# Kernel optimization log

Hardware: AMD Instinct MI355X
Metric: run time of the kernel (lower is better)

## Reference

```python
import jax, jax.numpy as jnp
import numpy as np

N_HEAD = 8
N_FEAT = 256
CHUNK = 64          # window/chunk size N
D_K = N_FEAT // N_HEAD
SCALE = D_K ** (-0.5)
B_ = 2048           # batch * nChunkNum
NCHUNK = 128        # nChunkNum (B_ % NCHUNK == 0)


def setup_inputs() -> dict:
    key = jax.random.key(0)
    ks = jax.random.split(key, 12)
    f32 = jnp.float32
    query = jax.random.normal(ks[0], (B_, CHUNK, N_FEAT), f32)
    key_t = jax.random.normal(ks[1], (B_, CHUNK, N_FEAT), f32)
    value = jax.random.normal(ks[2], (B_, CHUNK, N_FEAT), f32)
    # padding mask (B_, time2): multiplicative 0/1 floats
    mask = jax.random.randint(ks[3], (B_, CHUNK), 0, 2).astype(f32)
    # shifted-chunk additive mask (nChunkNum, N, N): 0 for neighbors, -100 otherwise
    cm_bin = jax.random.randint(ks[4], (NCHUNK, CHUNK, CHUNK), 0, 2)
    chunk_mask = jnp.where(cm_bin == 1, 0.0, -100.0).astype(f32)
    def lin(k):
        return jax.random.normal(k, (N_FEAT, N_FEAT), f32) * 0.02
    Wq, Wk, Wv, Wo = lin(ks[5]), lin(ks[6]), lin(ks[7]), lin(ks[8])
    bq = jnp.zeros((N_FEAT,), f32)
    bk = jnp.zeros((N_FEAT,), f32)
    bv = jnp.zeros((N_FEAT,), f32)
    bo = jnp.zeros((N_FEAT,), f32)
    rpb_table = jax.random.normal(ks[9], (2 * CHUNK - 1, N_HEAD), f32) * 0.02
    return {"query": query, "key": key_t, "value": value, "mask": mask,
            "chunk_mask": chunk_mask, "Wq": Wq, "bq": bq, "Wk": Wk, "bk": bk,
            "Wv": Wv, "bv": bv, "Wo": Wo, "bo": bo, "rpb_table": rpb_table}


def _rel_pos_index():
    # index[i, j] = (i - j) + CHUNK - 1, shape (N, N)
    w = jnp.arange(CHUNK)
    return w[:, None] - w[None, :] + (CHUNK - 1)


def reference(query, key, value, mask, chunk_mask, Wq, bq, Wk, bk, Wv, bv, Wo, bo, rpb_table):
    B, N, _ = query.shape
    # qkv projections -> (B, h, N, d_k)
    def proj(x, W, b):
        y = x @ W.T + b
        return y.reshape(B, N, N_HEAD, D_K).transpose(0, 2, 1, 3)
    q = proj(query, Wq, bq)
    k = proj(key, Wk, bk)
    v = proj(value, Wv, bv)
    # windowed attention scores (B, h, N, N)
    scores = jnp.einsum("bhid,bhjd->bhij", q, k) * SCALE
    # relative position bias: gather (N, N, h) -> (h, N, N)
    rpb = rpb_table[_rel_pos_index()].transpose(2, 0, 1)
    scores = scores + rpb[None]
    # padding mask: multiply, then fill zeros with -100 (as in torch source)
    scores = scores * mask[:, None, None, :]
    scores = jnp.where(scores == 0, jnp.float32(-100.0), scores)
    # additive shifted-chunk mask
    nC = chunk_mask.shape[0]
    scores = scores.reshape(B // nC, nC, N_HEAD, N, N) + chunk_mask[None, :, None]
    scores = scores.reshape(B, N_HEAD, N, N)
    attn = jax.nn.softmax(scores, axis=-1)
    x = jnp.einsum("bhij,bhjd->bhid", attn, v)          # (B, h, N, d_k)
    x = x.transpose(0, 2, 1, 3).reshape(B, N, N_FEAT)     # (B, N, n_feat)
    return x @ Wo.T + bo
```

## Files before the change

kernel.cpp:

```cpp
#include <hip/hip_runtime.h>
#include <hip/hip_bf16.h>

typedef __bf16 bf16_t;
typedef __bf16 bf16x8 __attribute__((ext_vector_type(8)));
typedef __bf16 bf16x4 __attribute__((ext_vector_type(4)));
typedef float f32x4 __attribute__((ext_vector_type(4)));

#define OFF_A   0
#define OFF_B   32768
#define OFF_RPB 65536
#define OFF_CMM (65536 + 4096)
#define OFF_PAD (65536 + 4096 + 512)
#define SMEM_BYTES (65536 + 4096 + 512 + 8)

__device__ __forceinline__ int tile_off(int r, int c) {
  return (r << 9) + ((((c >> 3) ^ (r & 7)) << 4) | ((c & 7) << 1));
}
__device__ __forceinline__ int vt_off(int d, int j) {
  return (d << 7) + ((((j >> 3) ^ (d & 7)) << 4) | ((j & 7) << 1));
}
__device__ __forceinline__ int ps_off(int i, int j) {
  return (i << 6) + ((((j >> 3) ^ ((i >> 1) & 3)) << 4) | ((j & 7) << 1));
}

template <int UNROLL>
__device__ __forceinline__ void stage_x(const float* __restrict__ src, char* __restrict__ dst, int tid) {
  const float4* s4 = (const float4*)src;
#pragma unroll
  for (int kk = 0; kk < 8; kk += UNROLL) {
    float4 v[UNROLL];
#pragma unroll
    for (int u = 0; u < UNROLL; ++u) v[u] = s4[tid + ((kk + u) << 9)];
#pragma unroll
    for (int u = 0; u < UNROLL; ++u) {
      int f = tid + ((kk + u) << 9);
      int row = f >> 6;
      int col = (f & 63) << 2;
      bf16x4 p;
      p[0] = (bf16_t)v[u].x; p[1] = (bf16_t)v[u].y; p[2] = (bf16_t)v[u].z; p[3] = (bf16_t)v[u].w;
      *(bf16x4*)(dst + tile_off(row, col)) = p;
    }
  }
}

__device__ __forceinline__ void gemm_tile(const char* __restrict__ sA, const bf16_t* __restrict__ W,
                                          int cb, int l15, int g, f32x4 acc[4][2]) {
#pragma unroll
  for (int kt = 0; kt < 8; ++kt) {
    bf16x8 a[4];
#pragma unroll
    for (int mt = 0; mt < 4; ++mt)
      a[mt] = *(const bf16x8*)(sA + tile_off(mt*16 + l15, kt*32 + g*8));
#pragma unroll
    for (int nt = 0; nt < 2; ++nt) {
      bf16x8 bw = *(const bf16x8*)(W + (cb + nt*16 + l15)*256 + kt*32 + g*8);
#pragma unroll
      for (int mt = 0; mt < 4; ++mt)
        acc[mt][nt] = __builtin_amdgcn_mfma_f32_16x16x32_bf16(a[mt], bw, acc[mt][nt], 0, 0, 0);
    }
  }
}

__device__ __forceinline__ void gemm_tile2(const char* __restrict__ sA, const char* __restrict__ sB,
                                           const bf16_t* __restrict__ W0, const bf16_t* __restrict__ W1,
                                           int cb, int l15, int g,
                                           f32x4 acc0[4][2], f32x4 acc1[4][2]) {
  const bf16_t* w0p = W0 + (cb + l15)*256 + g*8;
  const bf16_t* w1p = W1 + (cb + l15)*256 + g*8;
#pragma unroll
  for (int kt = 0; kt < 8; ++kt) {
    bf16x8 a0[4], a1[4];
#pragma unroll
    for (int mt = 0; mt < 4; ++mt) {
      a0[mt] = *(const bf16x8*)(sA + tile_off(mt*16 + l15, kt*32 + g*8));
      a1[mt] = *(const bf16x8*)(sB + tile_off(mt*16 + l15, kt*32 + g*8));
    }
#pragma unroll
    for (int nt = 0; nt < 2; ++nt) {
      bf16x8 bw0 = *(const bf16x8*)(w0p + nt*16*256 + kt*32);
      bf16x8 bw1 = *(const bf16x8*)(w1p + nt*16*256 + kt*32);
#pragma unroll
      for (int mt = 0; mt < 4; ++mt) {
        acc0[mt][nt] = __builtin_amdgcn_mfma_f32_16x16x32_bf16(a0[mt], bw0, acc0[mt][nt], 0, 0, 0);
        acc1[mt][nt] = __builtin_amdgcn_mfma_f32_16x16x32_bf16(a1[mt], bw1, acc1[mt][nt], 0, 0, 0);
      }
    }
  }
}

__global__ __launch_bounds__(512, 2)
void chunk_attn_kernel(
    const float* __restrict__ qg, const float* __restrict__ kg, const float* __restrict__ vg,
    const float* __restrict__ maskg, const float* __restrict__ cmg,
    const float* __restrict__ bq, const float* __restrict__ bk, const float* __restrict__ bv,
    const float* __restrict__ bo, const float* __restrict__ rpbg,
    const bf16_t* __restrict__ Wb, float* __restrict__ outg) {
  extern __shared__ char sm[];
  char*  bufA  = sm + OFF_A;
  char*  bufB  = sm + OFF_B;
  float* sRpb  = (float*)(sm + OFF_RPB);
  char*  sCmm  = sm + OFF_CMM;

  const int b = blockIdx.x, tid = threadIdx.x;
  const int wave = tid >> 6, lane = tid & 63, l15 = lane & 15, g = lane >> 4;
  const int cb = wave << 5;
  char* scr = bufB + (wave << 12);

  for (int i = tid; i < 1016; i += 512) sRpb[((i & 7) << 7) + (i >> 3)] = rpbg[i];
  {
    if (wave == 0) {
      float mv = maskg[(b << 6) + lane];
      unsigned long long bm = __ballot(mv == 0.0f);
      if (lane == 0) *(unsigned long long*)(sm + OFF_PAD) = bm;
    }
    const float* cmb = cmg + ((size_t)(b & 127) << 12);
#pragma unroll
    for (int it = 0; it < 8; ++it) {
      int row = (wave << 3) + it;
      float cv = cmb[(row << 6) + lane];
      unsigned long long bm = __ballot(cv < -50.0f);
      if (lane == 0) *(unsigned long long*)(sCmm + (row << 3)) = bm;
    }
  }
  stage_x<4>(qg + (size_t)b*16384, bufA, tid);
  stage_x<4>(kg + (size_t)b*16384, bufB, tid);
  __syncthreads();

  {
    f32x4 qacc[4][2] = {}, kacc[4][2] = {};
    gemm_tile2(bufA, bufB, Wb + 0*65536, Wb + 1*65536, cb, l15, g, qacc, kacc);
    __syncthreads();
    float bq0 = bq[cb+l15], bq1 = bq[cb+16+l15];
    float bk0 = bk[cb+l15], bk1 = bk[cb+16+l15];
#pragma unroll
    for (int mt = 0; mt < 4; ++mt)
#pragma unroll
      for (int nt = 0; nt < 2; ++nt)
#pragma unroll
        for (int r = 0; r < 4; ++r) {
          int row = mt*16 + g*4 + r, col = cb + nt*16 + l15;
          *(bf16_t*)(bufA + tile_off(row, col)) = (bf16_t)(qacc[mt][nt][r] + (nt ? bq1 : bq0));
          *(bf16_t*)(bufB + tile_off(row, col)) = (bf16_t)(kacc[mt][nt][r] + (nt ? bk1 : bk0));
        }
  }
  __asm__ volatile("s_waitcnt lgkmcnt(0)" ::: "memory");

  f32x4 St[4][4];
  {
    bf16x8 ka[4], qb[4];
#pragma unroll
    for (int t = 0; t < 4; ++t) {
      ka[t] = *(const bf16x8*)(bufB + tile_off(t*16 + l15, cb + g*8));
      qb[t] = *(const bf16x8*)(bufA + tile_off(t*16 + l15, cb + g*8));
    }
    const f32x4 z = {};
#pragma unroll
    for (int mj = 0; mj < 4; ++mj)
#pragma unroll
      for (int ni = 0; ni < 4; ++ni)
        St[mj][ni] = __builtin_amdgcn_mfma_f32_16x16x32_bf16(ka[mj], qb[ni], z, 0, 0, 0);
  }

  const float* rpbw = sRpb + (wave << 7);
  unsigned long long padm = *(const unsigned long long*)(sm + OFF_PAD);
  unsigned int padl = (unsigned int)padm, padh = (unsigned int)(padm >> 32);
#pragma unroll
  for (int mj = 0; mj < 4; ++mj) {
    unsigned int pw = (mj >= 2) ? padh : padl;
#pragma unroll
    for (int ni = 0; ni < 4; ++ni) {
      int i = ni*16 + l15;
      unsigned long long cmm = *(const unsigned long long*)(sCmm + (i << 3));
      unsigned int cw = (mj >= 2) ? (unsigned int)(cmm >> 32) : (unsigned int)cmm;
#pragma unroll
      for (int r = 0; r < 4; ++r) {
        int j = mj*16 + g*4 + r;
        int sh = j & 31;
        float s1 = St[mj][ni][r] * 0.17677669529663689f + rpbw[i - j + 63];
        float base = ((pw >> sh) & 1u) ? -100.0f : s1;
        St[mj][ni][r] = ((cw >> sh) & 1u) ? base - 100.0f : base;
      }
    }
  }

  float rinv[4];
  bf16x4 pbf[4][4];
#pragma unroll
  for (int ni = 0; ni < 4; ++ni) {
    float m = -1e30f;
#pragma unroll
    for (int mj = 0; mj < 4; ++mj)
#pragma unroll
      for (int r = 0; r < 4; ++r) m = fmaxf(m, St[mj][ni][r]);
    m = fmaxf(m, __shfl_xor(m, 16));
    m = fmaxf(m, __shfl_xor(m, 32));
    float s = 0.0f;
#pragma unroll
    for (int mj = 0; mj < 4; ++mj)
#pragma unroll
      for (int r = 0; r < 4; ++r) {
        float p = __expf(St[mj][ni][r] - m);
        pbf[mj][ni][r] = (bf16_t)p;
        s += p;
      }
    s += __shfl_xor(s, 16);
    s += __shfl_xor(s, 32);
    rinv[ni] = 1.0f / s;
  }

  __syncthreads();
  stage_x<4>(vg + (size_t)b*16384, bufB, tid);
  __syncthreads();

  {
    f32x4 vacc[4][2] = {};
    gemm_tile(bufB, Wb + 2*65536, cb, l15, g, vacc);
    float b0 = bv[cb+l15], b1 = bv[cb+16+l15];
#pragma unroll
    for (int nt = 0; nt < 2; ++nt)
#pragma unroll
      for (int mt = 0; mt < 4; ++mt) {
        bf16x4 p;
#pragma unroll
        for (int r = 0; r < 4; ++r) p[r] = (bf16_t)(vacc[mt][nt][r] + (nt ? b1 : b0));
        *(bf16x4*)(bufA + vt_off(cb + nt*16 + l15, mt*16 + g*4)) = p;
      }
  }
  __syncthreads();

  f32x4 Xa[2][4] = {};
#pragma unroll
  for (int h2 = 0; h2 < 2; ++h2) {
#pragma unroll
    for (int mj = 2*h2; mj < 2*h2 + 2; ++mj)
#pragma unroll
      for (int ni = 0; ni < 4; ++ni)
        *(bf16x4*)(scr + ps_off(ni*16 + l15, (mj & 1)*16 + g*4)) = pbf[mj][ni];
    __asm__ volatile("s_waitcnt lgkmcnt(0)" ::: "memory");
    bf16x8 va[2], pb[4];
#pragma unroll
    for (int mtd = 0; mtd < 2; ++mtd)
      va[mtd] = *(const bf16x8*)(bufA + vt_off(cb + mtd*16 + l15, h2*32 + g*8));
#pragma unroll
    for (int ni = 0; ni < 4; ++ni)
      pb[ni] = *(const bf16x8*)(scr + ps_off(ni*16 + l15, g*8));
#pragma unroll
    for (int mtd = 0; mtd < 2; ++mtd)
#pragma unroll
      for (int ni = 0; ni < 4; ++ni)
        Xa[mtd][ni] = __builtin_amdgcn_mfma_f32_16x16x32_bf16(va[mtd], pb[ni], Xa[mtd][ni], 0, 0, 0);
  }

  __syncthreads();
#pragma unroll
  for (int mtd = 0; mtd < 2; ++mtd)
#pragma unroll
    for (int ni = 0; ni < 4; ++ni)
#pragma unroll
      for (int r = 0; r < 4; ++r) {
        int dloc = mtd*16 + g*4 + r;
        int i = ni*16 + l15;
        *(bf16_t*)(bufB + tile_off(i, cb + dloc)) = (bf16_t)(Xa[mtd][ni][r] * rinv[ni]);
      }
  __syncthreads();

  {
    f32x4 acc[4][2] = {};
    gemm_tile(bufB, Wb + 3*65536, cb, l15, g, acc);
    float b0 = bo[cb+l15], b1 = bo[cb+16+l15];
    float* ob = outg + (size_t)b * 16384;
#pragma unroll
    for (int mt = 0; mt < 4; ++mt)
#pragma unroll
      for (int nt = 0; nt < 2; ++nt)
#pragma unroll
        for (int r = 0; r < 4; ++r)
          ob[(mt*16 + g*4 + r)*256 + cb + nt*16 + l15] = acc[mt][nt][r] + (nt ? b1 : b0);
  }
}

__global__ void cvt_weights(const float* __restrict__ Wq, const float* __restrict__ Wk,
                            const float* __restrict__ Wv, const float* __restrict__ Wo,
                            bf16_t* __restrict__ dst) {
  int idx = blockIdx.x * 256 + threadIdx.x;
  int which = idx >> 14;
  int off = idx & 16383;
  const float* src = (which == 0) ? Wq : (which == 1) ? Wk : (which == 2) ? Wv : Wo;
  float4 v = ((const float4*)src)[off];
  bf16x4 p;
  p[0] = (bf16_t)v.x; p[1] = (bf16_t)v.y; p[2] = (bf16_t)v.z; p[3] = (bf16_t)v.w;
  *(bf16x4*)(dst + which*65536 + off*4) = p;
}

extern "C" void kernel_launch(void* const* d_in, const int* in_sizes, int n_in,
                              void* d_out, int out_size, void* d_ws, size_t ws_size,
                              hipStream_t stream) {
  (void)in_sizes; (void)n_in; (void)out_size; (void)ws_size;
  const float* qg  = (const float*)d_in[0];
  const float* kg  = (const float*)d_in[1];
  const float* vg  = (const float*)d_in[2];
  const float* mg  = (const float*)d_in[3];
  const float* cmg = (const float*)d_in[4];
  const float* Wq  = (const float*)d_in[5];
  const float* bq  = (const float*)d_in[6];
  const float* Wk  = (const float*)d_in[7];
  const float* bk  = (const float*)d_in[8];
  const float* Wv  = (const float*)d_in[9];
  const float* bv  = (const float*)d_in[10];
  const float* Wo  = (const float*)d_in[11];
  const float* bo  = (const float*)d_in[12];
  const float* rpb = (const float*)d_in[13];
  bf16_t* Wb = (bf16_t*)d_ws;
  float* outg = (float*)d_out;

  hipFuncSetAttribute(reinterpret_cast<const void*>(chunk_attn_kernel),
                      hipFuncAttributeMaxDynamicSharedMemorySize, SMEM_BYTES);
  cvt_weights<<<256, 256, 0, stream>>>(Wq, Wk, Wv, Wo, Wb);
  chunk_attn_kernel<<<2048, 512, SMEM_BYTES, stream>>>(qg, kg, vg, mg, cmg,
      bq, bk, bv, bo, rpb, Wb, outg);
}
```

Measured before the change: 251.8 us.

## Fuse V projection into the QKV GEMM using a third LDS buffer

Stages Q, K and V into three separate LDS tiles up front and computes all three projections in one fused three-way GEMM loop, storing V transposed into its own buffer. This removes the later V staging phase, its separate GEMM and two block-wide barriers, and drops a barrier before the output write by moving the per-wave P scratch into the Q buffer. In exchange LDS use grows by 32 KB per block and the fused loop holds three accumulator sets at once. That likely prevents two 512-thread blocks from sharing a CU and raises register pressure.

```diff
diff --git a/kernel.cpp b/kernel.cpp
--- a/kernel.cpp
+++ b/kernel.cpp
@@ -8,10 +8,11 @@
 
 #define OFF_A   0
 #define OFF_B   32768
-#define OFF_RPB 65536
-#define OFF_CMM (65536 + 4096)
-#define OFF_PAD (65536 + 4096 + 512)
-#define SMEM_BYTES (65536 + 4096 + 512 + 8)
+#define OFF_C   65536
+#define OFF_RPB 98304
+#define OFF_CMM (98304 + 4096)
+#define OFF_PAD (98304 + 4096 + 512)
+#define SMEM_BYTES (98304 + 4096 + 512 + 8)
 
 __device__ __forceinline__ int tile_off(int r, int c) {
   return (r << 9) + ((((c >> 3) ^ (r & 7)) << 4) | ((c & 7) << 1));
@@ -45,6 +46,7 @@
 
 __device__ __forceinline__ void gemm_tile(const char* __restrict__ sA, const bf16_t* __restrict__ W,
                                           int cb, int l15, int g, f32x4 acc[4][2]) {
+  const bf16_t* wp = W + (cb + l15) * 256 + g * 8;
 #pragma unroll
   for (int kt = 0; kt < 8; ++kt) {
     bf16x8 a[4];
@@ -53,7 +55,7 @@
       a[mt] = *(const bf16x8*)(sA + tile_off(mt*16 + l15, kt*32 + g*8));
 #pragma unroll
     for (int nt = 0; nt < 2; ++nt) {
-      bf16x8 bw = *(const bf16x8*)(W + (cb + nt*16 + l15)*256 + kt*32 + g*8);
+      bf16x8 bw = *(const bf16x8*)(wp + nt * 16 * 256 + kt * 32);
 #pragma unroll
       for (int mt = 0; mt < 4; ++mt)
         acc[mt][nt] = __builtin_amdgcn_mfma_f32_16x16x32_bf16(a[mt], bw, acc[mt][nt], 0, 0, 0);
@@ -61,28 +63,35 @@
   }
 }
 
-__device__ __forceinline__ void gemm_tile2(const char* __restrict__ sA, const char* __restrict__ sB,
+__device__ __forceinline__ void gemm_tile3(const char* __restrict__ sA, const char* __restrict__ sB,
+                                           const char* __restrict__ sC,
                                            const bf16_t* __restrict__ W0, const bf16_t* __restrict__ W1,
+                                           const bf16_t* __restrict__ W2,
                                            int cb, int l15, int g,
-                                           f32x4 acc0[4][2], f32x4 acc1[4][2]) {
-  const bf16_t* w0p = W0 + (cb + l15)*256 + g*8;
-  const bf16_t* w1p = W1 + (cb + l15)*256 + g*8;
+                                           f32x4 acc0[4][2], f32x4 acc1[4][2], f32x4 acc2[4][2]) {
+  const bf16_t* w0p = W0 + (cb + l15) * 256 + g * 8;
+  const bf16_t* w1p = W1 + (cb + l15) * 256 + g * 8;
+  const bf16_t* w2p = W2 + (cb + l15) * 256 + g * 8;
 #pragma unroll
   for (int kt = 0; kt < 8; ++kt) {
-    bf16x8 a0[4], a1[4];
+    bf16x8 a0[4], a1[4], a2[4];
 #pragma unroll
     for (int mt = 0; mt < 4; ++mt) {
-      a0[mt] = *(const bf16x8*)(sA + tile_off(mt*16 + l15, kt*32 + g*8));
-      a1[mt] = *(const bf16x8*)(sB + tile_off(mt*16 + l15, kt*32 + g*8));
+      int off = tile_off(mt*16 + l15, kt*32 + g*8);
+      a0[mt] = *(const bf16x8*)(sA + off);
+      a1[mt] = *(const bf16x8*)(sB + off);
+      a2[mt] = *(const bf16x8*)(sC + off);
     }
 #pragma unroll
     for (int nt = 0; nt < 2; ++nt) {
-      bf16x8 bw0 = *(const bf16x8*)(w0p + nt*16*256 + kt*32);
-      bf16x8 bw1 = *(const bf16x8*)(w1p + nt*16*256 + kt*32);
+      bf16x8 bw0 = *(const bf16x8*)(w0p + nt * 16 * 256 + kt * 32);
+      bf16x8 bw1 = *(const bf16x8*)(w1p + nt * 16 * 256 + kt * 32);
+      bf16x8 bw2 = *(const bf16x8*)(w2p + nt * 16 * 256 + kt * 32);
 #pragma unroll
       for (int mt = 0; mt < 4; ++mt) {
         acc0[mt][nt] = __builtin_amdgcn_mfma_f32_16x16x32_bf16(a0[mt], bw0, acc0[mt][nt], 0, 0, 0);
         acc1[mt][nt] = __builtin_amdgcn_mfma_f32_16x16x32_bf16(a1[mt], bw1, acc1[mt][nt], 0, 0, 0);
+        acc2[mt][nt] = __builtin_amdgcn_mfma_f32_16x16x32_bf16(a2[mt], bw2, acc2[mt][nt], 0, 0, 0);
       }
     }
   }
@@ -98,13 +107,14 @@
   extern __shared__ char sm[];
   char*  bufA  = sm + OFF_A;
   char*  bufB  = sm + OFF_B;
+  char*  bufC  = sm + OFF_C;
   float* sRpb  = (float*)(sm + OFF_RPB);
   char*  sCmm  = sm + OFF_CMM;
 
   const int b = blockIdx.x, tid = threadIdx.x;
   const int wave = tid >> 6, lane = tid & 63, l15 = lane & 15, g = lane >> 4;
   const int cb = wave << 5;
-  char* scr = bufB + (wave << 12);
+  char* scr = bufA + (wave << 12);
 
   for (int i = tid; i < 1016; i += 512) sRpb[((i & 7) << 7) + (i >> 3)] = rpbg[i];
   {
@@ -124,11 +134,13 @@
   }
   stage_x<4>(qg + (size_t)b*16384, bufA, tid);
   stage_x<4>(kg + (size_t)b*16384, bufB, tid);
+  stage_x<4>(vg + (size_t)b*16384, bufC, tid);
   __syncthreads();
 
   {
-    f32x4 qacc[4][2] = {}, kacc[4][2] = {};
-    gemm_tile2(bufA, bufB, Wb + 0*65536, Wb + 1*65536, cb, l15, g, qacc, kacc);
+    f32x4 qacc[4][2] = {}, kacc[4][2] = {}, vacc[4][2] = {};
+    gemm_tile3(bufA, bufB, bufC, Wb + 0*65536, Wb + 1*65536, Wb + 2*65536,
+               cb, l15, g, qacc, kacc, vacc);
     __syncthreads();
     float bq0 = bq[cb+l15], bq1 = bq[cb+16+l15];
     float bk0 = bk[cb+l15], bk1 = bk[cb+16+l15];
@@ -142,6 +154,16 @@
           *(bf16_t*)(bufA + tile_off(row, col)) = (bf16_t)(qacc[mt][nt][r] + (nt ? bq1 : bq0));
           *(bf16_t*)(bufB + tile_off(row, col)) = (bf16_t)(kacc[mt][nt][r] + (nt ? bk1 : bk0));
         }
+    float bv0 = bv[cb+l15], bv1 = bv[cb+16+l15];
+#pragma unroll
+    for (int nt = 0; nt < 2; ++nt)
+#pragma unroll
+      for (int mt = 0; mt < 4; ++mt) {
+        bf16x4 p;
+#pragma unroll
+        for (int r = 0; r < 4; ++r) p[r] = (bf16_t)(vacc[mt][nt][r] + (nt ? bv1 : bv0));
+        *(bf16x4*)(bufC + vt_off(cb + nt*16 + l15, mt*16 + g*4)) = p;
+      }
   }
   __asm__ volatile("s_waitcnt lgkmcnt(0)" ::: "memory");
 
@@ -209,24 +231,6 @@
   }
 
   __syncthreads();
-  stage_x<4>(vg + (size_t)b*16384, bufB, tid);
-  __syncthreads();
-
-  {
-    f32x4 vacc[4][2] = {};
-    gemm_tile(bufB, Wb + 2*65536, cb, l15, g, vacc);
-    float b0 = bv[cb+l15], b1 = bv[cb+16+l15];
-#pragma unroll
-    for (int nt = 0; nt < 2; ++nt)
-#pragma unroll
-      for (int mt = 0; mt < 4; ++mt) {
-        bf16x4 p;
-#pragma unroll
-        for (int r = 0; r < 4; ++r) p[r] = (bf16_t)(vacc[mt][nt][r] + (nt ? b1 : b0));
-        *(bf16x4*)(bufA + vt_off(cb + nt*16 + l15, mt*16 + g*4)) = p;
-      }
-  }
-  __syncthreads();
 
   f32x4 Xa[2][4] = {};
 #pragma unroll
@@ -240,7 +244,7 @@
     bf16x8 va[2], pb[4];
 #pragma unroll
     for (int mtd = 0; mtd < 2; ++mtd)
-      va[mtd] = *(const bf16x8*)(bufA + vt_off(cb + mtd*16 + l15, h2*32 + g*8));
+      va[mtd] = *(const bf16x8*)(bufC + vt_off(cb + mtd*16 + l15, h2*32 + g*8));
 #pragma unroll
     for (int ni = 0; ni < 4; ++ni)
       pb[ni] = *(const bf16x8*)(scr + ps_off(ni*16 + l15, g*8));
@@ -251,7 +255,6 @@
         Xa[mtd][ni] = __builtin_amdgcn_mfma_f32_16x16x32_bf16(va[mtd], pb[ni], Xa[mtd][ni], 0, 0, 0);
   }
 
-  __syncthreads();
 #pragma unroll
   for (int mtd = 0; mtd < 2; ++mtd)
 #pragma unroll
```

Result: slower. 282.2 us (+12.1%).

## Split each head across two waves, doubling block size to 1024 threads

Applied to the files above, without the earlier changes.

Each head is now handled by two waves, each covering half of the rows (M tiles for the projections, query rows for attention), and the block grows from 512 to 1024 threads. Per-wave accumulators and register arrays shrink by half, which raises wave-level parallelism and should lower register pressure. In exchange, weight fragments are loaded twice per block (once by each wave of a pair), the cross-wave dependency on Q/K needs an extra full barrier in place of a waitcnt, and each wave's scratch region shrinks. Occupancy with 1024-thread blocks and 70KB of shared memory may be limited to one or two blocks per CU.

```diff
diff --git a/kernel.cpp b/kernel.cpp
--- a/kernel.cpp
+++ b/kernel.cpp
@@ -23,72 +23,68 @@
   return (i << 6) + ((((j >> 3) ^ ((i >> 1) & 3)) << 4) | ((j & 7) << 1));
 }
 
-template <int UNROLL>
 __device__ __forceinline__ void stage_x(const float* __restrict__ src, char* __restrict__ dst, int tid) {
   const float4* s4 = (const float4*)src;
 #pragma unroll
-  for (int kk = 0; kk < 8; kk += UNROLL) {
-    float4 v[UNROLL];
-#pragma unroll
-    for (int u = 0; u < UNROLL; ++u) v[u] = s4[tid + ((kk + u) << 9)];
-#pragma unroll
-    for (int u = 0; u < UNROLL; ++u) {
-      int f = tid + ((kk + u) << 9);
-      int row = f >> 6;
-      int col = (f & 63) << 2;
-      bf16x4 p;
-      p[0] = (bf16_t)v[u].x; p[1] = (bf16_t)v[u].y; p[2] = (bf16_t)v[u].z; p[3] = (bf16_t)v[u].w;
-      *(bf16x4*)(dst + tile_off(row, col)) = p;
-    }
-  }
-}
-
-__device__ __forceinline__ void gemm_tile(const char* __restrict__ sA, const bf16_t* __restrict__ W,
-                                          int cb, int l15, int g, f32x4 acc[4][2]) {
+  for (int k = 0; k < 4; ++k) {
+    int f = tid + (k << 10);
+    float4 v = s4[f];
+    int row = f >> 6;
+    int col = (f & 63) << 2;
+    bf16x4 p;
+    p[0] = (bf16_t)v.x; p[1] = (bf16_t)v.y; p[2] = (bf16_t)v.z; p[3] = (bf16_t)v.w;
+    *(bf16x4*)(dst + tile_off(row, col)) = p;
+  }
+}
+
+__device__ __forceinline__ void gemm_tileH(const char* __restrict__ sA, const bf16_t* __restrict__ W,
+                                           int cb, int mb, int l15, int g, f32x4 acc[2][2]) {
+  const bf16_t* wp = W + (cb + l15)*256 + g*8;
 #pragma unroll
   for (int kt = 0; kt < 8; ++kt) {
-    bf16x8 a[4];
-#pragma unroll
-    for (int mt = 0; mt < 4; ++mt)
-      a[mt] = *(const bf16x8*)(sA + tile_off(mt*16 + l15, kt*32 + g*8));
+    bf16x8 a[2];
+#pragma unroll
+    for (int mtl = 0; mtl < 2; ++mtl)
+      a[mtl] = *(const bf16x8*)(sA + tile_off((mb + mtl)*16 + l15, kt*32 + g*8));
 #pragma unroll
     for (int nt = 0; nt < 2; ++nt) {
-      bf16x8 bw = *(const bf16x8*)(W + (cb + nt*16 + l15)*256 + kt*32 + g*8);
-#pragma unroll
-      for (int mt = 0; mt < 4; ++mt)
-        acc[mt][nt] = __builtin_amdgcn_mfma_f32_16x16x32_bf16(a[mt], bw, acc[mt][nt], 0, 0, 0);
-    }
-  }
-}
-
-__device__ __forceinline__ void gemm_tile2(const char* __restrict__ sA, const char* __restrict__ sB,
-                                           const bf16_t* __restrict__ W0, const bf16_t* __restrict__ W1,
-                                           int cb, int l15, int g,
-                                           f32x4 acc0[4][2], f32x4 acc1[4][2]) {
+      bf16x8 bw = *(const bf16x8*)(wp + nt*16*256 + kt*32);
+#pragma unroll
+      for (int mtl = 0; mtl < 2; ++mtl)
+        acc[mtl][nt] = __builtin_amdgcn_mfma_f32_16x16x32_bf16(a[mtl], bw, acc[mtl][nt], 0, 0, 0);
+    }
+  }
+}
+
+__device__ __forceinline__ void gemm_tile2H(const char* __restrict__ sA, const char* __restrict__ sB,
+                                            const bf16_t* __restrict__ W0, const bf16_t* __restrict__ W1,
+                                            int cb, int mb, int l15, int g,
+                                            f32x4 acc0[2][2], f32x4 acc1[2][2]) {
   const bf16_t* w0p = W0 + (cb + l15)*256 + g*8;
   const bf16_t* w1p = W1 + (cb + l15)*256 + g*8;
 #pragma unroll
   for (int kt = 0; kt < 8; ++kt) {
-    bf16x8 a0[4], a1[4];
-#pragma unroll
-    for (int mt = 0; mt < 4; ++mt) {
-      a0[mt] = *(const bf16x8*)(sA + tile_off(mt*16 + l15, kt*32 + g*8));
-      a1[mt] = *(const bf16x8*)(sB + tile_off(mt*16 + l15, kt*32 + g*8));
+    bf16x8 a0[2], a1[2];
+#pragma unroll
+    for (int mtl = 0; mtl < 2; ++mtl) {
+      int off = tile_off((mb + mtl)*16 + l15, kt*32 + g*8);
+      a0[mtl] = *(const bf16x8*)(sA + off);
+      a1[mtl] = *(const bf16x8*)(sB + off);
     }
 #pragma unroll
     for (int nt = 0; nt < 2; ++nt) {
       bf16x8 bw0 = *(const bf16x8*)(w0p + nt*16*256 + kt*32);
       bf16x8 bw1 = *(const bf16x8*)(w1p + nt*16*256 + kt*32);
 #pragma unroll
-      for (int mt = 0; mt < 4; ++mt) {
-        acc0[mt][nt] = __builtin_amdgcn_mfma_f32_16x16x32_bf16(a0[mt], bw0, acc0[mt][nt], 0, 0, 0);
-        acc1[mt][nt] = __builtin_amdgcn_mfma_f32_16x16x32_bf16(a1[mt], bw1, acc1[mt][nt], 0, 0, 0);
-      }
-    }
-  }
-}
-
-__global__ __launch_bounds__(512, 2)
+      for (int mtl = 0; mtl < 2; ++mtl) {
+        acc0[mtl][nt] = __builtin_amdgcn_mfma_f32_16x16x32_bf16(a0[mtl], bw0, acc0[mtl][nt], 0, 0, 0);
+        acc1[mtl][nt] = __builtin_amdgcn_mfma_f32_16x16x32_bf16(a1[mtl], bw1, acc1[mtl][nt], 0, 0, 0);
+      }
+    }
+  }
+}
+
+__global__ __launch_bounds__(1024, 2)
 void chunk_attn_kernel(
     const float* __restrict__ qg, const float* __restrict__ kg, const float* __restrict__ vg,
     const float* __restrict__ maskg, const float* __restrict__ cmg,
@@ -103,10 +99,13 @@
 
   const int b = blockIdx.x, tid = threadIdx.x;
   const int wave = tid >> 6, lane = tid & 63, l15 = lane & 15, g = lane >> 4;
-  const int cb = wave << 5;
-  char* scr = bufB + (wave << 12);
-
-  for (int i = tid; i < 1016; i += 512) sRpb[((i & 7) << 7) + (i >> 3)] = rpbg[i];
+  const int head = wave >> 1, hh = wave & 1;
+  const int cb = head << 5;
+  const int mb = hh << 1;
+  const int nb = hh << 1;
+  char* scr = bufB + (wave << 11);
+
+  for (int i = tid; i < 1016; i += 1024) sRpb[((i & 7) << 7) + (i >> 3)] = rpbg[i];
   {
     if (wave == 0) {
       float mv = maskg[(b << 6) + lane];
@@ -115,83 +114,84 @@
     }
     const float* cmb = cmg + ((size_t)(b & 127) << 12);
 #pragma unroll
-    for (int it = 0; it < 8; ++it) {
-      int row = (wave << 3) + it;
+    for (int it = 0; it < 4; ++it) {
+      int row = (wave << 2) + it;
       float cv = cmb[(row << 6) + lane];
       unsigned long long bm = __ballot(cv < -50.0f);
       if (lane == 0) *(unsigned long long*)(sCmm + (row << 3)) = bm;
     }
   }
-  stage_x<4>(qg + (size_t)b*16384, bufA, tid);
-  stage_x<4>(kg + (size_t)b*16384, bufB, tid);
-  __syncthreads();
-
-  {
-    f32x4 qacc[4][2] = {}, kacc[4][2] = {};
-    gemm_tile2(bufA, bufB, Wb + 0*65536, Wb + 1*65536, cb, l15, g, qacc, kacc);
+  stage_x(qg + (size_t)b*16384, bufA, tid);
+  stage_x(kg + (size_t)b*16384, bufB, tid);
+  __syncthreads();
+
+  {
+    f32x4 qacc[2][2] = {}, kacc[2][2] = {};
+    gemm_tile2H(bufA, bufB, Wb + 0*65536, Wb + 1*65536, cb, mb, l15, g, qacc, kacc);
     __syncthreads();
     float bq0 = bq[cb+l15], bq1 = bq[cb+16+l15];
     float bk0 = bk[cb+l15], bk1 = bk[cb+16+l15];
 #pragma unroll
-    for (int mt = 0; mt < 4; ++mt)
+    for (int mtl = 0; mtl < 2; ++mtl)
 #pragma unroll
       for (int nt = 0; nt < 2; ++nt)
 #pragma unroll
         for (int r = 0; r < 4; ++r) {
-          int row = mt*16 + g*4 + r, col = cb + nt*16 + l15;
-          *(bf16_t*)(bufA + tile_off(row, col)) = (bf16_t)(qacc[mt][nt][r] + (nt ? bq1 : bq0));
-          *(bf16_t*)(bufB + tile_off(row, col)) = (bf16_t)(kacc[mt][nt][r] + (nt ? bk1 : bk0));
+          int row = (mb + mtl)*16 + g*4 + r, col = cb + nt*16 + l15;
+          *(bf16_t*)(bufA + tile_off(row, col)) = (bf16_t)(qacc[mtl][nt][r] + (nt ? bq1 : bq0));
+          *(bf16_t*)(bufB + tile_off(row, col)) = (bf16_t)(kacc[mtl][nt][r] + (nt ? bk1 : bk0));
         }
   }
-  __asm__ volatile("s_waitcnt lgkmcnt(0)" ::: "memory");
-
-  f32x4 St[4][4];
-  {
-    bf16x8 ka[4], qb[4];
-#pragma unroll
-    for (int t = 0; t < 4; ++t) {
+  __syncthreads();
+
+  f32x4 St[4][2];
+  {
+    bf16x8 ka[4], qb[2];
+#pragma unroll
+    for (int t = 0; t < 4; ++t)
       ka[t] = *(const bf16x8*)(bufB + tile_off(t*16 + l15, cb + g*8));
-      qb[t] = *(const bf16x8*)(bufA + tile_off(t*16 + l15, cb + g*8));
-    }
+#pragma unroll
+    for (int nl = 0; nl < 2; ++nl)
+      qb[nl] = *(const bf16x8*)(bufA + tile_off((nb + nl)*16 + l15, cb + g*8));
     const f32x4 z = {};
 #pragma unroll
     for (int mj = 0; mj < 4; ++mj)
 #pragma unroll
-      for (int ni = 0; ni < 4; ++ni)
-        St[mj][ni] = __builtin_amdgcn_mfma_f32_16x16x32_bf16(ka[mj], qb[ni], z, 0, 0, 0);
-  }
-
-  const float* rpbw = sRpb + (wave << 7);
+      for (int nl = 0; nl < 2; ++nl)
+        St[mj][nl] = __builtin_amdgcn_mfma_f32_16x16x32_bf16(ka[mj], qb[nl], z, 0, 0, 0);
+  }
+
+  const float* rpbw = sRpb + (head << 7);
   unsigned long long padm = *(const unsigned long long*)(sm + OFF_PAD);
   unsigned int padl = (unsigned int)padm, padh = (unsigned int)(padm >> 32);
 #pragma unroll
   for (int mj = 0; mj < 4; ++mj) {
     unsigned int pw = (mj >= 2) ? padh : padl;
 #pragma unroll
-    for (int ni = 0; ni < 4; ++ni) {
-      int i = ni*16 + l15;
+    for (int nl = 0; nl < 2; ++nl) {
+      int i = (nb + nl)*16 + l15;
       unsigned long long cmm = *(const unsigned long long*)(sCmm + (i << 3));
       unsigned int cw = (mj >= 2) ? (unsigned int)(cmm >> 32) : (unsigned int)cmm;
 #pragma unroll
       for (int r = 0; r < 4; ++r) {
         int j = mj*16 + g*4 + r;
         int sh = j & 31;
-        float s1 = St[mj][ni][r] * 0.17677669529663689f + rpbw[i - j + 63];
+        float s1 = St[mj][nl][r] * 0.17677669529663689f + rpbw[i - j + 63];
         float base = ((pw >> sh) & 1u) ? -100.0f : s1;
-        St[mj][ni][r] = ((cw >> sh) & 1u) ? base - 100.0f : base;
-      }
-    }
-  }
-
-  float rinv[4];
-  bf16x4 pbf[4][4];
-#pragma unroll
-  for (int ni = 0; ni < 4; ++ni) {
+        St[mj][nl][r] = ((cw >> sh) & 1u) ? base - 100.0f : base;
+      }
+    }
+  }
+
+  float rinv[2];
+  bf16x4 pbf[4][2];
+#pragma unroll
+  for (int nl = 0; nl < 2; ++nl) {
     float m = -1e30f;
 #pragma unroll
     for (int mj = 0; mj < 4; ++mj)
 #pragma unroll
-      for (int r = 0; r < 4; ++r) m = fmaxf(m, St[mj][ni][r]);
+      for (int r = 0; r < 4; ++r) m = fmaxf(m, St[mj][nl][r]);
     m = fmaxf(m, __shfl_xor(m, 16));
     m = fmaxf(m, __shfl_xor(m, 32));
     float s = 0.0f;
@@ -199,83 +199,83 @@
     for (int mj = 0; mj < 4; ++mj)
 #pragma unroll
       for (int r = 0; r < 4; ++r) {
-        float p = __expf(St[mj][ni][r] - m);
-        pbf[mj][ni][r] = (bf16_t)p;
+        float p = __expf(St[mj][nl][r] - m);
+        pbf[mj][nl][r] = (bf16_t)p;
         s += p;
       }
     s += __shfl_xor(s, 16);
     s += __shfl_xor(s, 32);
-    rinv[ni] = 1.0f / s;
-  }
-
-  __syncthreads();
-  stage_x<4>(vg + (size_t)b*16384, bufB, tid);
-  __syncthreads();
-
-  {
-    f32x4 vacc[4][2] = {};
-    gemm_tile(bufB, Wb + 2*65536, cb, l15, g, vacc);
+    rinv[nl] = 1.0f / s;
+  }
+
+  __syncthreads();
+  stage_x(vg + (size_t)b*16384, bufB, tid);
+  __syncthreads();
+
+  {
+    f32x4 vacc[2][2] = {};
+    gemm_tileH(bufB, Wb + 2*65536, cb, mb, l15, g, vacc);
     float b0 = bv[cb+l15], b1 = bv[cb+16+l15];
 #pragma unroll
     for (int nt = 0; nt < 2; ++nt)
 #pragma unroll
-      for (int mt = 0; mt < 4; ++mt) {
+      for (int mtl = 0; mtl < 2; ++mtl) {
         bf16x4 p;
 #pragma unroll
-        for (int r = 0; r < 4; ++r) p[r] = (bf16_t)(vacc[mt][nt][r] + (nt ? b1 : b0));
-        *(bf16x4*)(bufA + vt_off(cb + nt*16 + l15, mt*16 + g*4)) = p;
-      }
-  }
-  __syncthreads();
-
-  f32x4 Xa[2][4] = {};
+        for (int r = 0; r < 4; ++r) p[r] = (bf16_t)(vacc[mtl][nt][r] + (nt ? b1 : b0));
+        *(bf16x4*)(bufA + vt_off(cb + nt*16 + l15, (mb + mtl)*16 + g*4)) = p;
+      }
+  }
+  __syncthreads();
+
+  f32x4 Xa[2][2] = {};
 #pragma unroll
   for (int h2 = 0; h2 < 2; ++h2) {
 #pragma unroll
-    for (int mj = 2*h2; mj < 2*h2 + 2; ++mj)
-#pragma unroll
-      for (int ni = 0; ni < 4; ++ni)
-        *(bf16x4*)(scr + ps_off(ni*16 + l15, (mj & 1)*16 + g*4)) = pbf[mj][ni];
+    for (int mjl = 0; mjl < 2; ++mjl)
+#pragma unroll
+      for (int nl = 0; nl < 2; ++nl)
+        *(bf16x4*)(scr + ps_off(nl*16 + l15, mjl*16 + g*4)) = pbf[2*h2 + mjl][nl];
     __asm__ volatile("s_waitcnt lgkmcnt(0)" ::: "memory");
-    bf16x8 va[2], pb[4];
+    bf16x8 va[2], pb[2];
 #pragma unroll
     for (int mtd = 0; mtd < 2; ++mtd)
       va[mtd] = *(const bf16x8*)(bufA + vt_off(cb + mtd*16 + l15, h2*32 + g*8));
 #pragma unroll
-    for (int ni = 0; ni < 4; ++ni)
-      pb[ni] = *(const bf16x8*)(scr + ps_off(ni*16 + l15, g*8));
+    for (int nl = 0; nl < 2; ++nl)
+      pb[nl] = *(const bf16x8*)(scr + ps_off(nl*16 + l15, g*8));
 #pragma unroll
     for (int mtd = 0; mtd < 2; ++mtd)
 #pragma unroll
-      for (int ni = 0; ni < 4; ++ni)
-        Xa[mtd][ni] = __builtin_amdgcn_mfma_f32_16x16x32_bf16(va[mtd], pb[ni], Xa[mtd][ni], 0, 0, 0);
+      for (int nl = 0; nl < 2; ++nl)
+        Xa[mtd][nl] = __builtin_amdgcn_mfma_f32_16x16x32_bf16(va[mtd], pb[nl], Xa[mtd][nl], 0, 0, 0);
   }
 
   __syncthreads();
 #pragma unroll
   for (int mtd = 0; mtd < 2; ++mtd)
 #pragma unroll
-    for (int ni = 0; ni < 4; ++ni)
+    for (int nl = 0; nl < 2; ++nl)
 #pragma unroll
       for (int r = 0; r < 4; ++r) {
         int dloc = mtd*16 + g*4 + r;
-        int i = ni*16 + l15;
-        *(bf16_t*)(bufB + tile_off(i, cb + dloc)) = (bf16_t)(Xa[mtd][ni][r] * rinv[ni]);
-      }
-  __syncthreads();
-
-  {
-    f32x4 acc[4][2] = {};
-    gemm_tile(bufB, Wb + 3*65536, cb, l15, g, acc);
+        int i = (nb + nl)*16 + l15;
+        *(bf16_t*)(bufB + tile_off(i, cb + dloc)) = (bf16_t)(Xa[mtd][nl][r] * rinv[nl]);
+      }
+  __syncthreads();
+
+  {
+    f32x4 acc[2][2] = {};
+    gemm_tileH(bufB, Wb + 3*65536, cb, mb, l15, g, acc);
     float b0 = bo[cb+l15], b1 = bo[cb+16+l15];
     float* ob = outg + (size_t)b * 16384;
 #pragma unroll
-    for (int mt = 0; mt < 4; ++mt)
+    for (int mtl = 0; mtl < 2; ++mtl)
 #pragma unroll
       for (int nt = 0; nt < 2; ++nt)
 #pragma unroll
         for (int r = 0; r < 4; ++r)
-          ob[(mt*16 + g*4 + r)*256 + cb + nt*16 + l15] = acc[mt][nt][r] + (nt ? b1 : b0);
+          ob[((mb + mtl)*16 + g*4 + r)*256 + cb + nt*16 + l15] = acc[mtl][nt][r] + (nt ? b1 : b0);
   }
 }
 
@@ -316,6 +316,6 @@
   hipFuncSetAttribute(reinterpret_cast<const void*>(chunk_attn_kernel),
                       hipFuncAttributeMaxDynamicSharedMemorySize, SMEM_BYTES);
   cvt_weights<<<256, 256, 0, stream>>>(Wq, Wk, Wv, Wo, Wb);
-  chunk_attn_kernel<<<2048, 512, SMEM_BYTES, stream>>>(qg, kg, vg, mg, cmg,
+  chunk_attn_kernel<<<2048, 1024, SMEM_BYTES, stream>>>(qg, kg, vg, mg, cmg,
       bq, bk, bv, bo, rpb, Wb, outg);
 }
```

New measurement: 386.3 us. +53.4%, slower.

## Split fused chunk attention into separate QKV projection and attention kernels

Applied to the files above, without the earlier changes.

Adds a QKV projection kernel, launched with 6144 blocks, that writes bf16 Q and K into the output buffer and a transposed bf16 V into the workspace. A second attention kernel then loads these, runs masked softmax and P·V, and applies the output projection. The split targets the low occupancy of the single fused kernel: each stage gets a smaller register and shared-memory footprint and can run more waves per CU. The cost is extra global traffic to write and re-read the bf16 intermediates. The old fused kernel remains as a fallback when the workspace is too small.

```diff
diff --git a/kernel.cpp b/kernel.cpp
--- a/kernel.cpp
+++ b/kernel.cpp
@@ -5,13 +5,6 @@
 typedef __bf16 bf16x8 __attribute__((ext_vector_type(8)));
 typedef __bf16 bf16x4 __attribute__((ext_vector_type(4)));
 typedef float f32x4 __attribute__((ext_vector_type(4)));
-
-#define OFF_A   0
-#define OFF_B   32768
-#define OFF_RPB 65536
-#define OFF_CMM (65536 + 4096)
-#define OFF_PAD (65536 + 4096 + 512)
-#define SMEM_BYTES (65536 + 4096 + 512 + 8)
 
 __device__ __forceinline__ int tile_off(int r, int c) {
   return (r << 9) + ((((c >> 3) ^ (r & 7)) << 4) | ((c & 7) << 1));
@@ -45,6 +38,7 @@
 
 __device__ __forceinline__ void gemm_tile(const char* __restrict__ sA, const bf16_t* __restrict__ W,
                                           int cb, int l15, int g, f32x4 acc[4][2]) {
+  const bf16_t* wp = W + (cb + l15)*256 + g*8;
 #pragma unroll
   for (int kt = 0; kt < 8; ++kt) {
     bf16x8 a[4];
@@ -53,7 +47,7 @@
       a[mt] = *(const bf16x8*)(sA + tile_off(mt*16 + l15, kt*32 + g*8));
 #pragma unroll
     for (int nt = 0; nt < 2; ++nt) {
-      bf16x8 bw = *(const bf16x8*)(W + (cb + nt*16 + l15)*256 + kt*32 + g*8);
+      bf16x8 bw = *(const bf16x8*)(wp + nt*16*256 + kt*32);
 #pragma unroll
       for (int mt = 0; mt < 4; ++mt)
         acc[mt][nt] = __builtin_amdgcn_mfma_f32_16x16x32_bf16(a[mt], bw, acc[mt][nt], 0, 0, 0);
@@ -72,8 +66,9 @@
     bf16x8 a0[4], a1[4];
 #pragma unroll
     for (int mt = 0; mt < 4; ++mt) {
-      a0[mt] = *(const bf16x8*)(sA + tile_off(mt*16 + l15, kt*32 + g*8));
-      a1[mt] = *(const bf16x8*)(sB + tile_off(mt*16 + l15, kt*32 + g*8));
+      int off = tile_off(mt*16 + l15, kt*32 + g*8);
+      a0[mt] = *(const bf16x8*)(sA + off);
+      a1[mt] = *(const bf16x8*)(sB + off);
     }
 #pragma unroll
     for (int nt = 0; nt < 2; ++nt) {
@@ -87,6 +82,233 @@
     }
   }
 }
+
+__global__ __launch_bounds__(512, 4)
+void qkv_proj_kernel(const float* __restrict__ qg, const float* __restrict__ kg,
+                     const float* __restrict__ vg,
+                     const float* __restrict__ bq, const float* __restrict__ bk,
+                     const float* __restrict__ bv,
+                     const bf16_t* __restrict__ Wb,
+                     char* __restrict__ qk_out, char* __restrict__ vt_out) {
+  __shared__ char buf[32768];
+  const int bid = blockIdx.x;
+  const int which = bid >> 11;
+  const int b = bid & 2047;
+  const float* src  = (which == 0) ? qg : (which == 1) ? kg : vg;
+  const float* bias = (which == 0) ? bq : (which == 1) ? bk : bv;
+  const bf16_t* W = Wb + which * 65536;
+  const int tid = threadIdx.x, wave = tid >> 6, lane = tid & 63, l15 = lane & 15, g = lane >> 4;
+  const int cb = wave << 5;
+
+  stage_x<4>(src + (size_t)b * 16384, buf, tid);
+  __syncthreads();
+  f32x4 acc[4][2] = {};
+  gemm_tile(buf, W, cb, l15, g, acc);
+  __syncthreads();
+  float b0 = bias[cb + l15], b1 = bias[cb + 16 + l15];
+  if (which < 2) {
+#pragma unroll
+    for (int mt = 0; mt < 4; ++mt)
+#pragma unroll
+      for (int nt = 0; nt < 2; ++nt)
+#pragma unroll
+        for (int r = 0; r < 4; ++r)
+          *(bf16_t*)(buf + tile_off(mt*16 + g*4 + r, cb + nt*16 + l15)) =
+              (bf16_t)(acc[mt][nt][r] + (nt ? b1 : b0));
+  } else {
+#pragma unroll
+    for (int nt = 0; nt < 2; ++nt)
+#pragma unroll
+      for (int mt = 0; mt < 4; ++mt) {
+        bf16x4 p;
+#pragma unroll
+        for (int r = 0; r < 4; ++r) p[r] = (bf16_t)(acc[mt][nt][r] + (nt ? b1 : b0));
+        *(bf16x4*)(buf + vt_off(cb + nt*16 + l15, mt*16 + g*4)) = p;
+      }
+  }
+  __syncthreads();
+  char* dst = (which < 2) ? (qk_out + (size_t)b * 65536 + which * 32768)
+                          : (vt_out + (size_t)b * 32768);
+  const float4* s = (const float4*)buf;
+  float4* d = (float4*)dst;
+#pragma unroll
+  for (int k = 0; k < 4; ++k) d[tid + (k << 9)] = s[tid + (k << 9)];
+}
+
+#define A_OFF_RPB 65536
+#define A_OFF_CMM (65536 + 4096)
+#define A_OFF_PAD (65536 + 4096 + 512)
+#define A_SMEM (65536 + 4096 + 512 + 8)
+
+__global__ __launch_bounds__(512)
+__attribute__((amdgpu_waves_per_eu(4, 4)))
+void attn_kernel(const char* __restrict__ qk_in, const char* __restrict__ vt_in,
+                 const float* __restrict__ maskg, const float* __restrict__ cmg,
+                 const float* __restrict__ bo, const float* __restrict__ rpbg,
+                 const bf16_t* __restrict__ Wb, float* __restrict__ outg) {
+  extern __shared__ char sm[];
+  char*  bufA  = sm;
+  char*  bufB  = sm + 32768;
+  float* sRpb  = (float*)(sm + A_OFF_RPB);
+  char*  sCmm  = sm + A_OFF_CMM;
+
+  const int b = blockIdx.x, tid = threadIdx.x;
+  const int wave = tid >> 6, lane = tid & 63, l15 = lane & 15, g = lane >> 4;
+  const int cb = wave << 5;
+
+  for (int i = tid; i < 1016; i += 512) sRpb[((i & 7) << 7) + (i >> 3)] = rpbg[i];
+  {
+    if (wave == 0) {
+      float mv = maskg[(b << 6) + lane];
+      unsigned long long bm = __ballot(mv == 0.0f);
+      if (lane == 0) *(unsigned long long*)(sm + A_OFF_PAD) = bm;
+    }
+    const float* cmb = cmg + ((size_t)(b & 127) << 12);
+#pragma unroll
+    for (int it = 0; it < 8; ++it) {
+      int row = (wave << 3) + it;
+      float cv = cmb[(row << 6) + lane];
+      unsigned long long bm = __ballot(cv < -50.0f);
+      if (lane == 0) *(unsigned long long*)(sCmm + (row << 3)) = bm;
+    }
+  }
+  {
+    const float4* qs = (const float4*)(qk_in + (size_t)b * 65536);
+    float4* da = (float4*)bufA;
+    float4* db = (float4*)bufB;
+#pragma unroll
+    for (int k = 0; k < 4; ++k) {
+      da[tid + (k << 9)] = qs[tid + (k << 9)];
+      db[tid + (k << 9)] = qs[2048 + tid + (k << 9)];
+    }
+  }
+  __syncthreads();
+
+  const float* rpbw = sRpb + (wave << 7);
+  unsigned long long padm = *(const unsigned long long*)(sm + A_OFF_PAD);
+  unsigned int padl = (unsigned int)padm, padh = (unsigned int)(padm >> 32);
+  float rinv[4];
+  bf16x4 pbf[4][4];
+#pragma unroll
+  for (int half = 0; half < 2; ++half) {
+    f32x4 Sh[4][2];
+    {
+      bf16x8 qb0 = *(const bf16x8*)(bufA + tile_off((2*half + 0)*16 + l15, cb + g*8));
+      bf16x8 qb1 = *(const bf16x8*)(bufA + tile_off((2*half + 1)*16 + l15, cb + g*8));
+      const f32x4 z = {};
+#pragma unroll
+      for (int mj = 0; mj < 4; ++mj) {
+        bf16x8 ka = *(const bf16x8*)(bufB + tile_off(mj*16 + l15, cb + g*8));
+        Sh[mj][0] = __builtin_amdgcn_mfma_f32_16x16x32_bf16(ka, qb0, z, 0, 0, 0);
+        Sh[mj][1] = __builtin_amdgcn_mfma_f32_16x16x32_bf16(ka, qb1, z, 0, 0, 0);
+      }
+    }
+#pragma unroll
+    for (int nih = 0; nih < 2; ++nih) {
+      int ni = 2*half + nih;
+      int i = ni*16 + l15;
+      unsigned long long cmm = *(const unsigned long long*)(sCmm + (i << 3));
+      unsigned int cml = (unsigned int)cmm, cmh = (unsigned int)(cmm >> 32);
+      float m = -1e30f;
+#pragma unroll
+      for (int mj = 0; mj < 4; ++mj) {
+        unsigned int cw = (mj >= 2) ? cmh : cml;
+        unsigned int pw = (mj >= 2) ? padh : padl;
+#pragma unroll
+        for (int r = 0; r < 4; ++r) {
+          int j = mj*16 + g*4 + r;
+          int sh = j & 31;
+          float s1 = Sh[mj][nih][r] * 0.17677669529663689f + rpbw[i - j + 63];
+          float base = ((pw >> sh) & 1u) ? -100.0f : s1;
+          float sc = ((cw >> sh) & 1u) ? base - 100.0f : base;
+          Sh[mj][nih][r] = sc;
+          m = fmaxf(m, sc);
+        }
+      }
+      m = fmaxf(m, __shfl_xor(m, 16));
+      m = fmaxf(m, __shfl_xor(m, 32));
+      float s = 0.0f;
+#pragma unroll
+      for (int mj = 0; mj < 4; ++mj)
+#pragma unroll
+        for (int r = 0; r < 4; ++r) {
+          float p = __expf(Sh[mj][nih][r] - m);
+          pbf[mj][ni][r] = (bf16_t)p;
+          s += p;
+        }
+      s += __shfl_xor(s, 16);
+      s += __shfl_xor(s, 32);
+      rinv[ni] = 1.0f / s;
+    }
+  }
+
+  __syncthreads();
+  {
+    const float4* vs = (const float4*)(vt_in + (size_t)b * 32768);
+    float4* da = (float4*)bufA;
+#pragma unroll
+    for (int k = 0; k < 4; ++k) da[tid + (k << 9)] = vs[tid + (k << 9)];
+  }
+  __syncthreads();
+
+  char* scr = bufB + (wave << 12);
+  f32x4 Xa[2][4] = {};
+#pragma unroll
+  for (int h2 = 0; h2 < 2; ++h2) {
+#pragma unroll
+    for (int mj = 2*h2; mj < 2*h2 + 2; ++mj)
+#pragma unroll
+      for (int ni = 0; ni < 4; ++ni)
+        *(bf16x4*)(scr + ps_off(ni*16 + l15, (mj & 1)*16 + g*4)) = pbf[mj][ni];
+    __asm__ volatile("s_waitcnt lgkmcnt(0)" ::: "memory");
+    bf16x8 va[2], pb[4];
+#pragma unroll
+    for (int mtd = 0; mtd < 2; ++mtd)
+      va[mtd] = *(const bf16x8*)(bufA + vt_off(cb + mtd*16 + l15, h2*32 + g*8));
+#pragma unroll
+    for (int ni = 0; ni < 4; ++ni)
+      pb[ni] = *(const bf16x8*)(scr + ps_off(ni*16 + l15, g*8));
+#pragma unroll
+    for (int mtd = 0; mtd < 2; ++mtd)
+#pragma unroll
+      for (int ni = 0; ni < 4; ++ni)
+        Xa[mtd][ni] = __builtin_amdgcn_mfma_f32_16x16x32_bf16(va[mtd], pb[ni], Xa[mtd][ni], 0, 0, 0);
+  }
+
+  __syncthreads();
+#pragma unroll
+  for (int mtd = 0; mtd < 2; ++mtd)
+#pragma unroll
+    for (int ni = 0; ni < 4; ++ni)
+#pragma unroll
+      for (int r = 0; r < 4; ++r) {
+        int dloc = mtd*16 + g*4 + r;
+        int i = ni*16 + l15;
+        *(bf16_t*)(bufA + tile_off(i, cb + dloc)) = (bf16_t)(Xa[mtd][ni][r] * rinv[ni]);
+      }
+  __syncthreads();
+
+  {
+    f32x4 acc[4][2] = {};
+    gemm_tile(bufA, Wb + 3*65536, cb, l15, g, acc);
+    float b0 = bo[cb+l15], b1 = bo[cb+16+l15];
+    float* ob = outg + (size_t)b * 16384;
+#pragma unroll
+    for (int mt = 0; mt < 4; ++mt)
+#pragma unroll
+      for (int nt = 0; nt < 2; ++nt)
+#pragma unroll
+        for (int r = 0; r < 4; ++r)
+          ob[(mt*16 + g*4 + r)*256 + cb + nt*16 + l15] = acc[mt][nt][r] + (nt ? b1 : b0);
+  }
+}
+
+#define OFF_A   0
+#define OFF_B   32768
+#define OFF_RPB 65536
+#define OFF_CMM (65536 + 4096)
+#define OFF_PAD (65536 + 4096 + 512)
+#define SMEM_BYTES (65536 + 4096 + 512 + 8)
 
 __global__ __launch_bounds__(512, 2)
 void chunk_attn_kernel(
@@ -295,7 +517,7 @@
 extern "C" void kernel_launch(void* const* d_in, const int* in_sizes, int n_in,
                               void* d_out, int out_size, void* d_ws, size_t ws_size,
                               hipStream_t stream) {
-  (void)in_sizes; (void)n_in; (void)out_size; (void)ws_size;
+  (void)in_sizes; (void)n_in; (void)out_size;
   const float* qg  = (const float*)d_in[0];
   const float* kg  = (const float*)d_in[1];
   const float* vg  = (const float*)d_in[2];
@@ -313,9 +535,22 @@
   bf16_t* Wb = (bf16_t*)d_ws;
   float* outg = (float*)d_out;
 
-  hipFuncSetAttribute(reinterpret_cast<const void*>(chunk_attn_kernel),
-                      hipFuncAttributeMaxDynamicSharedMemorySize, SMEM_BYTES);
+  const size_t WS_NEEDED = 524288 + (size_t)2048 * 32768;
+
   cvt_weights<<<256, 256, 0, stream>>>(Wq, Wk, Wv, Wo, Wb);
-  chunk_attn_kernel<<<2048, 512, SMEM_BYTES, stream>>>(qg, kg, vg, mg, cmg,
-      bq, bk, bv, bo, rpb, Wb, outg);
-}
+
+  if (ws_size >= WS_NEEDED) {
+    char* vt_ws = (char*)d_ws + 524288;
+    qkv_proj_kernel<<<6144, 512, 0, stream>>>(qg, kg, vg, bq, bk, bv, Wb,
+                                              (char*)d_out, vt_ws);
+    hipFuncSetAttribute(reinterpret_cast<const void*>(attn_kernel),
+                        hipFuncAttributeMaxDynamicSharedMemorySize, A_SMEM);
+    attn_kernel<<<2048, 512, A_SMEM, stream>>>((const char*)d_out, vt_ws,
+                                               mg, cmg, bo, rpb, Wb, outg);
+  } else {
+    hipFuncSetAttribute(reinterpret_cast<const void*>(chunk_attn_kernel),
+                        hipFuncAttributeMaxDynamicSharedMemorySize, SMEM_BYTES);
+    chunk_attn_kernel<<<2048, 512, SMEM_BYTES, stream>>>(qg, kg, vg, mg, cmg,
+        bq, bk, bv, bo, rpb, Wb, outg);
+  }
+}
```

Result: slower. 276.5 us (+9.8%).
